# Performance work log

Measured on AMD Instinct MI355X. Metric: run time of the kernel, lower is better.

The kernel has to match this reference:

```python
import jax, jax.numpy as jnp
import numpy as np

N = 50000      # nodes
E = 800000     # edges (before self loops)
IN = 128       # in_channels
H = 4          # heads
C = 32         # hidden_channels (per head)
D = H * C      # concat output dim = 128
NEG_SLOPE = 0.2
LN_EPS = 1e-5


def setup_inputs() -> dict:
    key = jax.random.key(0)
    ks = jax.random.split(key, 24)
    def p(k, shape, s=0.1):
        return jax.random.normal(k, shape, dtype=jnp.float32) * s
    inp = {
        "x": p(ks[0], (N, IN), 1.0),
        "edge_index": jax.random.randint(ks[1], (2, E), 0, N, dtype=jnp.int32),
    }
    i = 2
    for l, ind in [(0, IN), (1, D)]:
        inp[f"Wl{l}"] = p(ks[i], (ind, D)); i += 1
        inp[f"bl{l}"] = p(ks[i], (D,), 0.02); i += 1
        inp[f"Wr{l}"] = p(ks[i], (ind, D)); i += 1
        inp[f"br{l}"] = p(ks[i], (D,), 0.02); i += 1
        inp[f"att{l}"] = p(ks[i], (H, C)); i += 1
        inp[f"Wres{l}"] = p(ks[i], (ind, D)); i += 1
        inp[f"bias{l}"] = p(ks[i], (D,), 0.02); i += 1
        inp[f"g{l}"] = jnp.ones((D,), jnp.float32)
        inp[f"be{l}"] = jnp.zeros((D,), jnp.float32)
    return inp


def _gatv2_layer(x, src, dst, Wl, bl, Wr, br, att, Wres, bias):
    """GATv2Conv with concat heads, add_self_loops already applied, residual."""
    n = x.shape[0]
    xl = (x @ Wl + bl).reshape(n, H, C)   # source transform
    xr = (x @ Wr + br).reshape(n, H, C)   # target transform
    # edge-level attention logits: e = a . LeakyReLU(xl[j] + xr[i])  [E, H]
    eh = jax.nn.leaky_relu(xl[src] + xr[dst], negative_slope=NEG_SLOPE)  # [E,H,C]
    score = jnp.einsum('ehc,hc->eh', eh, att)                            # [E,H]
    # segment softmax over incoming edges of each destination node
    smax = jax.ops.segment_max(score, dst, num_segments=n)               # [N,H]
    ex = jnp.exp(score - smax[dst])
    ssum = jax.ops.segment_sum(ex, dst, num_segments=n)                  # [N,H]
    alpha = ex / ssum[dst]                                               # [E,H]
    msg = xl[src] * alpha[:, :, None]                                    # [E,H,C]
    out = jax.ops.segment_sum(msg, dst, num_segments=n).reshape(n, D)
    return out + x @ Wres + bias  # residual (bias=False linear) + final bias


def _layernorm_relu(x, g, b):
    mu = jnp.mean(x, axis=-1, keepdims=True)
    var = jnp.mean(jnp.square(x - mu), axis=-1, keepdims=True)
    return jax.nn.relu((x - mu) * jax.lax.rsqrt(var + LN_EPS) * g + b)


def reference(x, edge_index,
              Wl0, bl0, Wr0, br0, att0, Wres0, bias0, g0, be0,
              Wl1, bl1, Wr1, br1, att1, Wres1, bias1, g1, be1):
    n = x.shape[0]
    loops = jnp.arange(n, dtype=edge_index.dtype)
    src = jnp.concatenate([edge_index[0], loops])  # add_self_loops=True
    dst = jnp.concatenate([edge_index[1], loops])
    h = _gatv2_layer(x, src, dst, Wl0, bl0, Wr0, br0, att0, Wres0, bias0)
    h = _layernorm_relu(h, g0, be0)
    h = _gatv2_layer(h, src, dst, Wl1, bl1, Wr1, br1, att1, Wres1, bias1)
    h = _layernorm_relu(h, g1, be1)
    return h
```

## Files before the change

kernel.cpp:

```cpp
#include <hip/hip_runtime.h>
#include <math.h>

#define D 128
#define LRELU 0.2f
#define LN_EPS 1e-5f
#define INV_LN2 1.4426950408889634f

#define NBMAX 512
#define CAP 4096
#define P1CHUNK 8192

typedef __attribute__((ext_vector_type(8))) short short8;
typedef __attribute__((ext_vector_type(8))) unsigned short ushort8;
typedef __attribute__((ext_vector_type(4))) float f32x4;
typedef __attribute__((ext_vector_type(2))) float f32x2;
typedef __attribute__((ext_vector_type(2))) unsigned int u32x2;
typedef __attribute__((ext_vector_type(4))) unsigned int u32x4;

static __device__ __forceinline__ unsigned short f2bf(float f) {
    union { float f; unsigned u; } a; a.f = f;
    unsigned r = a.u + 0x7FFFu + ((a.u >> 16) & 1u);
    return (unsigned short)(r >> 16);
}

static __device__ __forceinline__ f32x2 pk_add(f32x2 a, f32x2 b) {
    f32x2 d; asm("v_pk_add_f32 %0, %1, %2" : "=v"(d) : "v"(a), "v"(b)); return d;
}
static __device__ __forceinline__ f32x2 pk_mul(f32x2 a, f32x2 b) {
    f32x2 d; asm("v_pk_mul_f32 %0, %1, %2" : "=v"(d) : "v"(a), "v"(b)); return d;
}
static __device__ __forceinline__ f32x2 pk_fma(f32x2 a, f32x2 b, f32x2 c) {
    f32x2 d; asm("v_pk_fma_f32 %0, %1, %2, %3" : "=v"(d) : "v"(a), "v"(b), "v"(c)); return d;
}
static __device__ __forceinline__ f32x2 pk_abs(f32x2 a) {
    u32x2 u = __builtin_bit_cast(u32x2, a);
    u &= 0x7FFFFFFFu;
    return __builtin_bit_cast(f32x2, u);
}
static __device__ __forceinline__ f32x2 bf2x(unsigned u) {
    f32x2 r;
    r.x = __uint_as_float(u << 16);
    r.y = __uint_as_float(u & 0xFFFF0000u);
    return r;
}

static __device__ __forceinline__ float red4_dpp(float p) {
    int v = __builtin_amdgcn_update_dpp(0, __builtin_bit_cast(int, p), 0xB1, 0xf, 0xf, true);
    p += __builtin_bit_cast(float, v);
    v = __builtin_amdgcn_update_dpp(0, __builtin_bit_cast(int, p), 0x4E, 0xf, 0xf, true);
    p += __builtin_bit_cast(float, v);
    return p;
}

#define SCB 256


__global__ __launch_bounds__(256) void k_prep(
    const int* __restrict__ srcp, const int* __restrict__ dstp,
    int* __restrict__ bcur, unsigned* __restrict__ ebuf, int E, int N,
    const float* __restrict__ X, ushort* __restrict__ Xb, int Mp,
    const float* __restrict__ W0, const float* __restrict__ W1, const float* __restrict__ W2,
    const float* __restrict__ W3, const float* __restrict__ W4, const float* __restrict__ W5,
    ushort* __restrict__ Wp, int nP1, int nCV)
{
    const int bx = blockIdx.x;
    const int tid = threadIdx.x;
    if (bx < nP1) {
        __shared__ int h[NBMAX];
        const int E2 = E + N;
        const int e0 = bx * P1CHUNK;
        const int e1 = min(e0 + P1CHUNK, E2);
        for (int t = tid; t < NBMAX; t += 256) h[t] = 0;
        __syncthreads();
        for (int e = e0 + tid; e < e1; e += 256) {
            int d = (e < E) ? dstp[e] : e - E;
            atomicAdd(&h[d >> 7], 1);
        }
        __syncthreads();
        for (int b = tid; b < NBMAX; b += 256) {
            int c = h[b];
            h[b] = c ? atomicAdd(&bcur[b], c) : 0;
        }
        __syncthreads();
        for (int e = e0 + tid; e < e1; e += 256) {
            int d  = (e < E) ? dstp[e] : e - E;
            int sc = (e < E) ? srcp[e] : e - E;
            int b = d >> 7;
            int pos = atomicAdd(&h[b], 1) & (CAP - 1);
            ebuf[(size_t)b * CAP + pos] = ((unsigned)sc << 7) | (unsigned)(d & 127);
        }
    } else if (bx < nP1 + nCV) {
        int idx = (bx - nP1) * 256 + tid;
        if (idx >= Mp * (D / 4)) return;
        ushort4 o;
        if (idx < N * (D / 4)) {
            float4 v = ((const float4*)X)[idx];
            o.x = f2bf(v.x); o.y = f2bf(v.y); o.z = f2bf(v.z); o.w = f2bf(v.w);
        } else {
            o = make_ushort4(0, 0, 0, 0);
        }
        ((ushort4*)Xb)[idx] = o;
    } else {
        int bid = bx - nP1 - nCV;
        int m = bid >> 6;
        int o = ((bid & 63) << 8) + tid;
        const float* W;
        if (m == 0) W = W0; else if (m == 1) W = W1; else if (m == 2) W = W2;
        else if (m == 3) W = W3; else if (m == 4) W = W4; else W = W5;
        int j  = o & 7;
        int l  = (o >> 3) & 63;
        int ct = (o >> 9) & 7;
        int kc = o >> 12;
        int k   = kc * 32 + ((l >> 4) << 3) + j;
        int col = (ct << 4) + (l & 15);
        Wp[m * 16384 + o] = f2bf(W[k * D + col]);
    }
}


__global__ __launch_bounds__(256) void bhist_kernel(const unsigned* __restrict__ ebuf,
                                                    const int* __restrict__ bcur,
                                                    int* __restrict__ deg,
                                                    int* __restrict__ btot, int N) {
    const int b = blockIdx.x;
    const int base = b << 7;
    const int tid = threadIdx.x;
    __shared__ int h[128];
    __shared__ int t2[2];
    if (tid < 128) h[tid] = 0;
    __syncthreads();
    const int cnt = min(bcur[b], CAP);
    for (int k = tid; k < cnt; k += 256) {
        unsigned v = ebuf[(size_t)b * CAP + k];
        atomicAdd(&h[v & 127], 1);
    }
    __syncthreads();
    int v = (tid < 128) ? h[tid] : 0;
    if (tid < 128 && base + tid < N) deg[base + tid] = v;
    #pragma unroll
    for (int o = 32; o >= 1; o >>= 1) v += __shfl_xor(v, o);
    if (tid == 0)  t2[0] = v;
    if (tid == 64) t2[1] = v;
    __syncthreads();
    if (tid == 0) btot[b] = t2[0] + t2[1];
}


static __device__ __forceinline__ void gemm_body(
    int bxg, int seg, int tid,
    const ushort* __restrict__ Xb, const ushort* __restrict__ Wp,
    const float* __restrict__ bl, const float* __restrict__ br,
    ushort* __restrict__ XLb, ushort* __restrict__ XRb, ushort* __restrict__ RESb)
{
    const int l = tid & 63;
    const int wave = tid >> 6;
    const int wr = wave >> 1, wc = wave & 1;
    const int brow = bxg * 128 + wr * 64;
    const ushort* W = Wp + seg * 16384;

    f32x4 acc[4][4] = {};
    const int arow = brow + (l & 15);
    const int koff = (l >> 4) * 8;

    #pragma unroll
    for (int kc = 0; kc < 4; ++kc) {
        short8 A[4], B[4];
        #pragma unroll
        for (int at = 0; at < 4; ++at)
            A[at] = *(const short8*)&Xb[(size_t)(arow + at * 16) * D + kc * 32 + koff];
        #pragma unroll
        for (int ct = 0; ct < 4; ++ct) {
            int ctg = wc * 4 + ct;
            B[ct] = *(const short8*)&W[(((kc * 8 + ctg) * 64) + l) * 8];
        }
        #pragma unroll
        for (int at = 0; at < 4; ++at)
            #pragma unroll
            for (int ct = 0; ct < 4; ++ct)
                acc[at][ct] = __builtin_amdgcn_mfma_f32_16x16x32_bf16(A[at], B[ct], acc[at][ct], 0, 0, 0);
    }

    const int c = l & 15;
    const int r0 = (l >> 4) * 4;
    const float* bias = (seg == 0) ? bl : ((seg == 1) ? br : nullptr);
    #pragma unroll
    for (int ct = 0; ct < 4; ++ct) {
        int gcol = wc * 64 + ct * 16 + c;
        float bv = bias ? bias[gcol] : 0.f;
        #pragma unroll
        for (int at = 0; at < 4; ++at) {
            #pragma unroll
            for (int r = 0; r < 4; ++r) {
                int grow = brow + at * 16 + r0 + r;
                float v = acc[at][ct][r] + bv;
                size_t off = (size_t)grow * D + gcol;
                if (seg == 0)      XLb[off]  = f2bf(v);
                else if (seg == 1) XRb[off]  = f2bf(v);
                else               RESb[off] = f2bf(v);
            }
        }
    }
}


__global__ __launch_bounds__(256) void k_mid(
    const unsigned* __restrict__ ebuf, const int* __restrict__ bcur,
    const int* __restrict__ deg, const int* __restrict__ btot,
    int* __restrict__ off, int* __restrict__ csrc, int N, int NB, int nblk,
    const ushort* __restrict__ Xb, const ushort* __restrict__ Wp,
    const float* __restrict__ bl, const float* __restrict__ br,
    ushort* __restrict__ XLb, ushort* __restrict__ XRb, ushort* __restrict__ RESb)
{
    const int bx = blockIdx.x;
    if (bx < NB) {
        const int b = bx;
        const int base = b << 7;
        const int tid = threadIdx.x;
        __shared__ int cur[128];
        __shared__ int wsum[4];
        __shared__ int wtot[2];

        int acc = 0;
        for (int t = tid; t < b; t += 256) acc += btot[t];
        #pragma unroll
        for (int o = 32; o >= 1; o >>= 1) acc += __shfl_xor(acc, o);
        if ((tid & 63) == 0) wsum[tid >> 6] = acc;
        __syncthreads();
        const int B = wsum[0] + wsum[1] + wsum[2] + wsum[3];

        int dv = 0;
        if (tid < 128 && base + tid < N) dv = deg[base + tid];
        int incl = dv;
        if (tid < 128) {
            #pragma unroll
            for (int o = 1; o < 64; o <<= 1) {
                int u = __shfl_up(incl, o);
                if ((tid & 63) >= o) incl += u;
            }
        }
        if (tid == 63)  wtot[0] = incl;
        if (tid == 127) wtot[1] = incl;
        __syncthreads();
        if (tid < 128) {
            int add = (tid >= 64) ? wtot[0] : 0;
            int excl = B + add + incl - dv;
            cur[tid] = excl;
            if (base + tid < N) off[base + tid] = excl;
        }
        if (b == NB - 1 && tid == 0) off[N] = B + wtot[0] + wtot[1];
        __syncthreads();

        const int cnt = min(bcur[b], CAP);
        for (int k = tid; k < cnt; k += 256) {
            unsigned v = ebuf[(size_t)b * CAP + k];
            int p = atomicAdd(&cur[v & 127], 1);
            csrc[p] = v >> 7;
        }
    } else {
        int bid = bx - NB;
        int seg = bid / nblk;
        int bxg = bid - seg * nblk;
        gemm_body(bxg, seg, threadIdx.x, Xb, Wp, bl, br, XLb, XRb, RESb);
    }
}

__global__ __launch_bounds__(256) void gemm_mfma(
    const ushort* __restrict__ Xb, const ushort* __restrict__ Wp,
    const float* __restrict__ bl, const float* __restrict__ br,
    ushort* __restrict__ XLb, ushort* __restrict__ XRb, ushort* __restrict__ RESb)
{
    gemm_body(blockIdx.x, blockIdx.y, threadIdx.x, Xb, Wp, bl, br, XLb, XRb, RESb);
}


__global__ __launch_bounds__(256) void gat_node(
    const ushort* __restrict__ XLb, const ushort* __restrict__ XRb, const ushort* __restrict__ RESb,
    const float* __restrict__ att, const float* __restrict__ bias,
    const float* __restrict__ g, const float* __restrict__ be,
    const int* __restrict__ off, const int* __restrict__ csrc,
    float* __restrict__ OUTf, ushort* __restrict__ OUTb)
{
    const int l = threadIdx.x & 63;
    const int i = blockIdx.x * 16 + (threadIdx.x >> 6) * 4 + (l >> 4);
    const int f = (l & 15) * 8;
    const unsigned ibase = ((unsigned)i << 7) + f;
    const int lb = l & 48;

    f32x2 at06[4], at04[4];
    #pragma unroll
    for (int k = 0; k < 4; ++k) {
        float2 a = *(const float2*)&att[f + k * 2];
        f32x2 av; av.x = a.x; av.y = a.y;
        at06[k] = av * (0.6f * INV_LN2);
        at04[k] = av * (0.4f * INV_LN2);
    }

    u32x4 xru = __builtin_nontemporal_load((const u32x4*)&XRb[ibase]);
    f32x2 xr2[4];
    xr2[0] = bf2x(xru.x); xr2[1] = bf2x(xru.y); xr2[2] = bf2x(xru.z); xr2[3] = bf2x(xru.w);

    const int e0 = off[i], e1 = off[i + 1];
    const int len = e1 - e0;
    int mx = max(len, __shfl_xor(len, 16));
    mx = max(mx, __shfl_xor(mx, 32));

    float mA = -1e30f, sA = 0.f;
    float mB = -1e30f, sB = 0.f;
    f32x2 aA[4] = {};
    f32x2 aB[4] = {};

    for (int c0 = 0; c0 < mx; c0 += 16) {
        int myj = __builtin_nontemporal_load(&csrc[min(e0 + c0 + (l & 15), e1 - 1)]);
        const int rem = mx - c0;
        const int nbb = min(4, (rem + 3) >> 2);
        const int kleft = len - c0;

        u32x4 u_[4];
        {
            int s0 = __shfl(myj, lb + 0);
            int s1 = __shfl(myj, lb + 1);
            int s2 = __shfl(myj, lb + 2);
            int s3 = __shfl(myj, lb + 3);
            u_[0] = *(const u32x4*)&XLb[((unsigned)s0 << 7) + f];
            u_[1] = *(const u32x4*)&XLb[((unsigned)s1 << 7) + f];
            u_[2] = *(const u32x4*)&XLb[((unsigned)s2 << 7) + f];
            u_[3] = *(const u32x4*)&XLb[((unsigned)s3 << 7) + f];
        }

        #pragma unroll
        for (int bb = 0; bb < 4; ++bb) {
            if (bb >= nbb) break;
            u32x4 uc[4];
            #pragma unroll
            for (int j = 0; j < 4; ++j) uc[j] = u_[j];
            if (bb + 1 < nbb) {
                int s0 = __shfl(myj, lb + (bb + 1) * 4 + 0);
                int s1 = __shfl(myj, lb + (bb + 1) * 4 + 1);
                int s2 = __shfl(myj, lb + (bb + 1) * 4 + 2);
                int s3 = __shfl(myj, lb + (bb + 1) * 4 + 3);
                u_[0] = *(const u32x4*)&XLb[((unsigned)s0 << 7) + f];
                u_[1] = *(const u32x4*)&XLb[((unsigned)s1 << 7) + f];
                u_[2] = *(const u32x4*)&XLb[((unsigned)s2 << 7) + f];
                u_[3] = *(const u32x4*)&XLb[((unsigned)s3 << 7) + f];
            }

            const int kb = kleft - bb * 4;
            f32x2 xp[4][4];
            float p[4];
            #pragma unroll
            for (int j = 0; j < 4; ++j) {
                xp[j][0] = bf2x(uc[j].x);
                xp[j][1] = bf2x(uc[j].y);
                xp[j][2] = bf2x(uc[j].z);
                xp[j][3] = bf2x(uc[j].w);
                f32x2 v0 = pk_add(xp[j][0], xr2[0]);
                f32x2 pj2 = pk_mul(v0, at06[0]);
                pj2 = pk_fma(pk_abs(v0), at04[0], pj2);
                #pragma unroll
                for (int k = 1; k < 4; ++k) {
                    f32x2 v = pk_add(xp[j][k], xr2[k]);
                    pj2 = pk_fma(v, at06[k], pj2);
                    pj2 = pk_fma(pk_abs(v), at04[k], pj2);
                }
                float pj = pj2.x + pj2.y;
                pj = red4_dpp(pj);
                p[j] = (j < kb) ? pj : -1e30f;
            }
            float m0 = (bb & 1) ? mB : mA;
            float s0v = (bb & 1) ? sB : sA;
            float pmax = fmaxf(fmaxf(p[0], p[1]), fmaxf(p[2], p[3]));
            float nm = fmaxf(m0, pmax);
            float so = exp2f(m0 - nm);
            float w0 = exp2f(p[0] - nm), w1 = exp2f(p[1] - nm);
            float w2 = exp2f(p[2] - nm), w3 = exp2f(p[3] - nm);
            w0 = (0 < kb) ? w0 : 0.f;
            w1 = (1 < kb) ? w1 : 0.f;
            w2 = (2 < kb) ? w2 : 0.f;
            w3 = (3 < kb) ? w3 : 0.f;
            float sn = s0v * so + ((w0 + w1) + (w2 + w3));
            f32x2 so2; so2.x = so; so2.y = so;
            f32x2 w02; w02.x = w0; w02.y = w0;
            f32x2 w12; w12.x = w1; w12.y = w1;
            f32x2 w22; w22.x = w2; w22.y = w2;
            f32x2 w32; w32.x = w3; w32.y = w3;
            if (bb & 1) {
                #pragma unroll
                for (int k = 0; k < 4; ++k) {
                    f32x2 t = pk_mul(xp[0][k], w02);
                    t = pk_fma(xp[1][k], w12, t);
                    t = pk_fma(xp[2][k], w22, t);
                    t = pk_fma(xp[3][k], w32, t);
                    aB[k] = pk_fma(aB[k], so2, t);
                }
                mB = nm; sB = sn;
            } else {
                #pragma unroll
                for (int k = 0; k < 4; ++k) {
                    f32x2 t = pk_mul(xp[0][k], w02);
                    t = pk_fma(xp[1][k], w12, t);
                    t = pk_fma(xp[2][k], w22, t);
                    t = pk_fma(xp[3][k], w32, t);
                    aA[k] = pk_fma(aA[k], so2, t);
                }
                mA = nm; sA = sn;
            }
        }
    }

    float nmv = fmaxf(mA, mB);
    float soA = exp2f(mA - nmv);
    float soB = exp2f(mB - nmv);
    float s = sA * soA + sB * soB;
    f32x2 soA2; soA2.x = soA; soA2.y = soA;
    f32x2 soB2; soB2.x = soB; soB2.y = soB;
    f32x2 a2[4];
    #pragma unroll
    for (int k = 0; k < 4; ++k)
        a2[k] = pk_add(pk_mul(aA[k], soA2), pk_mul(aB[k], soB2));

    u32x4 ru = __builtin_nontemporal_load((const u32x4*)&RESb[ibase]);
    f32x2 rs2[4];
    rs2[0] = bf2x(ru.x); rs2[1] = bf2x(ru.y); rs2[2] = bf2x(ru.z); rs2[3] = bf2x(ru.w);
    const float4 biA = *(const float4*)&bias[f];
    const float4 biB = *(const float4*)&bias[f + 4];
    float inv = 1.f / s;
    float r0 = a2[0].x * inv + rs2[0].x + biA.x;
    float r1 = a2[0].y * inv + rs2[0].y + biA.y;
    float r2 = a2[1].x * inv + rs2[1].x + biA.z;
    float r3 = a2[1].y * inv + rs2[1].y + biA.w;
    float r4 = a2[2].x * inv + rs2[2].x + biB.x;
    float r5 = a2[2].y * inv + rs2[2].y + biB.y;
    float r6 = a2[3].x * inv + rs2[3].x + biB.z;
    float r7 = a2[3].y * inv + rs2[3].y + biB.w;

    float sum = ((r0 + r1) + (r2 + r3)) + ((r4 + r5) + (r6 + r7));
    float sq  = ((r0 * r0 + r1 * r1) + (r2 * r2 + r3 * r3))
              + ((r4 * r4 + r5 * r5) + (r6 * r6 + r7 * r7));
    #pragma unroll
    for (int o = 8; o >= 1; o >>= 1) {
        sum += __shfl_xor(sum, o);
        sq  += __shfl_xor(sq, o);
    }
    float mu  = sum * (1.f / 128.f);
    float var = sq * (1.f / 128.f) - mu * mu;
    float isd = rsqrtf(var + LN_EPS);
    const float4 gvA = *(const float4*)&g[f];
    const float4 gvB = *(const float4*)&g[f + 4];
    const float4 bvA = *(const float4*)&be[f];
    const float4 bvB = *(const float4*)&be[f + 4];
    float o0 = fmaxf((r0 - mu) * isd * gvA.x + bvA.x, 0.f);
    float o1 = fmaxf((r1 - mu) * isd * gvA.y + bvA.y, 0.f);
    float o2 = fmaxf((r2 - mu) * isd * gvA.z + bvA.z, 0.f);
    float o3 = fmaxf((r3 - mu) * isd * gvA.w + bvA.w, 0.f);
    float o4 = fmaxf((r4 - mu) * isd * gvB.x + bvB.x, 0.f);
    float o5 = fmaxf((r5 - mu) * isd * gvB.y + bvB.y, 0.f);
    float o6 = fmaxf((r6 - mu) * isd * gvB.z + bvB.z, 0.f);
    float o7 = fmaxf((r7 - mu) * isd * gvB.w + bvB.w, 0.f);

    if (OUTb) {
        ushort8 ob;
        ob[0] = f2bf(o0); ob[1] = f2bf(o1); ob[2] = f2bf(o2); ob[3] = f2bf(o3);
        ob[4] = f2bf(o4); ob[5] = f2bf(o5); ob[6] = f2bf(o6); ob[7] = f2bf(o7);
        __builtin_nontemporal_store(ob, (ushort8*)&OUTb[ibase]);
    } else {
        f32x4 oA; oA.x = o0; oA.y = o1; oA.z = o2; oA.w = o3;
        f32x4 oB; oB.x = o4; oB.y = o5; oB.z = o6; oB.w = o7;
        __builtin_nontemporal_store(oA, (f32x4*)&OUTf[ibase]);
        __builtin_nontemporal_store(oB, (f32x4*)&OUTf[ibase + 4]);
    }
}


extern "C" void kernel_launch(void* const* d_in, const int* in_sizes, int n_in,
                              void* d_out, int out_size, void* d_ws, size_t ws_size,
                              hipStream_t stream)
{
    const float* x    = (const float*)d_in[0];
    const int*   ei   = (const int*)d_in[1];
    const float* Wl0  = (const float*)d_in[2];
    const float* bl0  = (const float*)d_in[3];
    const float* Wr0  = (const float*)d_in[4];
    const float* br0  = (const float*)d_in[5];
    const float* att0 = (const float*)d_in[6];
    const float* Wres0= (const float*)d_in[7];
    const float* bias0= (const float*)d_in[8];
    const float* g0   = (const float*)d_in[9];
    const float* be0  = (const float*)d_in[10];
    const float* Wl1  = (const float*)d_in[11];
    const float* bl1  = (const float*)d_in[12];
    const float* Wr1  = (const float*)d_in[13];
    const float* br1  = (const float*)d_in[14];
    const float* att1 = (const float*)d_in[15];
    const float* Wres1= (const float*)d_in[16];
    const float* bias1= (const float*)d_in[17];
    const float* g1   = (const float*)d_in[18];
    const float* be1  = (const float*)d_in[19];

    const int N  = in_sizes[0] / D;
    const int E  = in_sizes[1] / 2;
    const int E2 = E + N;
    const int nblk = (N + 127) / 128;
    const int Mp = nblk * 128;
    const int NB = nblk;

    char* w = (char*)d_ws;
    ushort* Xb   = (ushort*)w; w += (size_t)Mp * D * 2;
    ushort* Hb   = (ushort*)w; w += (size_t)Mp * D * 2;
    ushort* XLb  = (ushort*)w; w += (size_t)Mp * D * 2;
    ushort* XRb  = (ushort*)w; w += (size_t)Mp * D * 2;
    ushort* RESb = (ushort*)w; w += (size_t)Mp * D * 2;
    ushort* Wp   = (ushort*)w; w += (size_t)6 * 16384 * 2;
    int* deg     = (int*)w; w += (size_t)N * 4;
    int* off     = (int*)w; w += (size_t)(N + 1) * 4;
    int* bcur    = (int*)w; w += (size_t)NBMAX * 4;
    int* btot    = (int*)w; w += (size_t)NBMAX * 4;
    unsigned* ebuf = (unsigned*)w; w += (size_t)NB * CAP * 4;
    int* csrc    = (int*)w; w += (size_t)E2 * 4;

    const int* srcp = ei;
    const int* dstp = ei + E;

    const int nP1 = (E2 + P1CHUNK - 1) / P1CHUNK;
    const int nCV = (Mp * (D / 4) + 255) / 256;
    const int nPW = 6 * 64;
    const int nGM = nblk * 3;

    hipMemsetAsync(bcur, 0, (size_t)NBMAX * 4, stream);
    k_prep<<<nP1 + nCV + nPW, 256, 0, stream>>>(srcp, dstp, bcur, ebuf, E, N,
                                                x, Xb, Mp,
                                                Wl0, Wr0, Wres0, Wl1, Wr1, Wres1,
                                                Wp, nP1, nCV);
    bhist_kernel<<<NB, 256, 0, stream>>>(ebuf, bcur, deg, btot, N);

    k_mid<<<NB + nGM, 256, 0, stream>>>(ebuf, bcur, deg, btot, off, csrc, N, NB, nblk,
                                        Xb, Wp, bl0, br0, XLb, XRb, RESb);

    const int gatg = N / 16;
    dim3 ggrid(nblk, 3);

    gat_node<<<gatg, 256, 0, stream>>>(XLb, XRb, RESb, att0, bias0, g0, be0, off, csrc, nullptr, Hb);
    gemm_mfma<<<ggrid, 256, 0, stream>>>(Hb, Wp + 3 * 16384, bl1, br1, XLb, XRb, RESb);
    gat_node<<<gatg, 256, 0, stream>>>(XLb, XRb, RESb, att1, bias1, g1, be1, off, csrc, (float*)d_out, nullptr);
}
```

Baseline: 185.1 us.

## Fold bucket histogram into CSR build and merge dual softmax accumulators

Removes the separate bhist_kernel launch. Each k_mid bucket block now builds its own per-node degree histogram from ebuf in shared memory and takes bucket prefix totals straight from bcur, which drops one launch and the deg/btot global round trips. The GAT node kernel also replaces the two alternating online-softmax accumulator sets (A/B) with a single running max/sum/accumulator, cutting registers and the final merge. The trade-off is a longer serial dependency chain in the softmax loop. Prefix sums from bcur ignore the CAP clamp, which differs from before only if a bucket overflows.

```diff
diff --git a/kernel.cpp b/kernel.cpp
--- a/kernel.cpp
+++ b/kernel.cpp
@@ -51,8 +51,6 @@
     p += __builtin_bit_cast(float, v);
     return p;
 }
-
-#define SCB 256
 
 
 __global__ __launch_bounds__(256) void k_prep(
@@ -118,34 +116,6 @@
 }
 
 
-__global__ __launch_bounds__(256) void bhist_kernel(const unsigned* __restrict__ ebuf,
-                                                    const int* __restrict__ bcur,
-                                                    int* __restrict__ deg,
-                                                    int* __restrict__ btot, int N) {
-    const int b = blockIdx.x;
-    const int base = b << 7;
-    const int tid = threadIdx.x;
-    __shared__ int h[128];
-    __shared__ int t2[2];
-    if (tid < 128) h[tid] = 0;
-    __syncthreads();
-    const int cnt = min(bcur[b], CAP);
-    for (int k = tid; k < cnt; k += 256) {
-        unsigned v = ebuf[(size_t)b * CAP + k];
-        atomicAdd(&h[v & 127], 1);
-    }
-    __syncthreads();
-    int v = (tid < 128) ? h[tid] : 0;
-    if (tid < 128 && base + tid < N) deg[base + tid] = v;
-    #pragma unroll
-    for (int o = 32; o >= 1; o >>= 1) v += __shfl_xor(v, o);
-    if (tid == 0)  t2[0] = v;
-    if (tid == 64) t2[1] = v;
-    __syncthreads();
-    if (tid == 0) btot[b] = t2[0] + t2[1];
-}
-
-
 static __device__ __forceinline__ void gemm_body(
     int bxg, int seg, int tid,
     const ushort* __restrict__ Xb, const ushort* __restrict__ Wp,
@@ -205,7 +175,6 @@
 
 __global__ __launch_bounds__(256) void k_mid(
     const unsigned* __restrict__ ebuf, const int* __restrict__ bcur,
-    const int* __restrict__ deg, const int* __restrict__ btot,
     int* __restrict__ off, int* __restrict__ csrc, int N, int NB, int nblk,
     const ushort* __restrict__ Xb, const ushort* __restrict__ Wp,
     const float* __restrict__ bl, const float* __restrict__ br,
@@ -216,20 +185,29 @@
         const int b = bx;
         const int base = b << 7;
         const int tid = threadIdx.x;
+        const int cntN = min(128, N - base);
+        __shared__ int h[128];
         __shared__ int cur[128];
         __shared__ int wsum[4];
         __shared__ int wtot[2];
 
         int acc = 0;
-        for (int t = tid; t < b; t += 256) acc += btot[t];
+        for (int t = tid; t < b; t += 256) acc += bcur[t];
         #pragma unroll
         for (int o = 32; o >= 1; o >>= 1) acc += __shfl_xor(acc, o);
         if ((tid & 63) == 0) wsum[tid >> 6] = acc;
+        if (tid < 128) h[tid] = 0;
         __syncthreads();
         const int B = wsum[0] + wsum[1] + wsum[2] + wsum[3];
 
-        int dv = 0;
-        if (tid < 128 && base + tid < N) dv = deg[base + tid];
+        const int cnt = min(bcur[b], CAP);
+        for (int k = tid; k < cnt; k += 256) {
+            unsigned v = ebuf[(size_t)b * CAP + k];
+            atomicAdd(&h[v & 127], 1);
+        }
+        __syncthreads();
+
+        int dv = (tid < 128) ? h[tid] : 0;
         int incl = dv;
         if (tid < 128) {
             #pragma unroll
@@ -245,12 +223,11 @@
             int add = (tid >= 64) ? wtot[0] : 0;
             int excl = B + add + incl - dv;
             cur[tid] = excl;
-            if (base + tid < N) off[base + tid] = excl;
+            if (tid < cntN) off[base + tid] = excl;
         }
         if (b == NB - 1 && tid == 0) off[N] = B + wtot[0] + wtot[1];
         __syncthreads();
 
-        const int cnt = min(bcur[b], CAP);
         for (int k = tid; k < cnt; k += 256) {
             unsigned v = ebuf[(size_t)b * CAP + k];
             int p = atomicAdd(&cur[v & 127], 1);
@@ -304,10 +281,8 @@
     int mx = max(len, __shfl_xor(len, 16));
     mx = max(mx, __shfl_xor(mx, 32));
 
-    float mA = -1e30f, sA = 0.f;
-    float mB = -1e30f, sB = 0.f;
-    f32x2 aA[4] = {};
-    f32x2 aB[4] = {};
+    float m = -1e30f, s = 0.f;
+    f32x2 a2[4] = {};
 
     for (int c0 = 0; c0 < mx; c0 += 16) {
         int myj = __builtin_nontemporal_load(&csrc[min(e0 + c0 + (l & 15), e1 - 1)]);
@@ -366,57 +341,28 @@
                 pj = red4_dpp(pj);
                 p[j] = (j < kb) ? pj : -1e30f;
             }
-            float m0 = (bb & 1) ? mB : mA;
-            float s0v = (bb & 1) ? sB : sA;
             float pmax = fmaxf(fmaxf(p[0], p[1]), fmaxf(p[2], p[3]));
-            float nm = fmaxf(m0, pmax);
-            float so = exp2f(m0 - nm);
+            float nm = fmaxf(m, pmax);
+            float so = exp2f(m - nm);
             float w0 = exp2f(p[0] - nm), w1 = exp2f(p[1] - nm);
             float w2 = exp2f(p[2] - nm), w3 = exp2f(p[3] - nm);
-            w0 = (0 < kb) ? w0 : 0.f;
-            w1 = (1 < kb) ? w1 : 0.f;
-            w2 = (2 < kb) ? w2 : 0.f;
-            w3 = (3 < kb) ? w3 : 0.f;
-            float sn = s0v * so + ((w0 + w1) + (w2 + w3));
+            s = s * so + ((w0 + w1) + (w2 + w3));
             f32x2 so2; so2.x = so; so2.y = so;
             f32x2 w02; w02.x = w0; w02.y = w0;
             f32x2 w12; w12.x = w1; w12.y = w1;
             f32x2 w22; w22.x = w2; w22.y = w2;
             f32x2 w32; w32.x = w3; w32.y = w3;
-            if (bb & 1) {
-                #pragma unroll
-                for (int k = 0; k < 4; ++k) {
-                    f32x2 t = pk_mul(xp[0][k], w02);
-                    t = pk_fma(xp[1][k], w12, t);
-                    t = pk_fma(xp[2][k], w22, t);
-                    t = pk_fma(xp[3][k], w32, t);
-                    aB[k] = pk_fma(aB[k], so2, t);
-                }
-                mB = nm; sB = sn;
-            } else {
-                #pragma unroll
-                for (int k = 0; k < 4; ++k) {
-                    f32x2 t = pk_mul(xp[0][k], w02);
-                    t = pk_fma(xp[1][k], w12, t);
-                    t = pk_fma(xp[2][k], w22, t);
-                    t = pk_fma(xp[3][k], w32, t);
-                    aA[k] = pk_fma(aA[k], so2, t);
-                }
-                mA = nm; sA = sn;
+            #pragma unroll
+            for (int k = 0; k < 4; ++k) {
+                f32x2 t = pk_mul(xp[0][k], w02);
+                t = pk_fma(xp[1][k], w12, t);
+                t = pk_fma(xp[2][k], w22, t);
+                t = pk_fma(xp[3][k], w32, t);
+                a2[k] = pk_fma(a2[k], so2, t);
             }
-        }
-    }
-
-    float nmv = fmaxf(mA, mB);
-    float soA = exp2f(mA - nmv);
-    float soB = exp2f(mB - nmv);
-    float s = sA * soA + sB * soB;
-    f32x2 soA2; soA2.x = soA; soA2.y = soA;
-    f32x2 soB2; soB2.x = soB; soB2.y = soB;
-    f32x2 a2[4];
-    #pragma unroll
-    for (int k = 0; k < 4; ++k)
-        a2[k] = pk_add(pk_mul(aA[k], soA2), pk_mul(aB[k], soB2));
+            m = nm;
+        }
+    }
 
     u32x4 ru = __builtin_nontemporal_load((const u32x4*)&RESb[ibase]);
     f32x2 rs2[4];
@@ -510,10 +456,8 @@
     ushort* XRb  = (ushort*)w; w += (size_t)Mp * D * 2;
     ushort* RESb = (ushort*)w; w += (size_t)Mp * D * 2;
     ushort* Wp   = (ushort*)w; w += (size_t)6 * 16384 * 2;
-    int* deg     = (int*)w; w += (size_t)N * 4;
     int* off     = (int*)w; w += (size_t)(N + 1) * 4;
     int* bcur    = (int*)w; w += (size_t)NBMAX * 4;
-    int* btot    = (int*)w; w += (size_t)NBMAX * 4;
     unsigned* ebuf = (unsigned*)w; w += (size_t)NB * CAP * 4;
     int* csrc    = (int*)w; w += (size_t)E2 * 4;
 
@@ -530,9 +474,8 @@
                                                 x, Xb, Mp,
                                                 Wl0, Wr0, Wres0, Wl1, Wr1, Wres1,
                                                 Wp, nP1, nCV);
-    bhist_kernel<<<NB, 256, 0, stream>>>(ebuf, bcur, deg, btot, N);
-
-    k_mid<<<NB + nGM, 256, 0, stream>>>(ebuf, bcur, deg, btot, off, csrc, N, NB, nblk,
+
+    k_mid<<<NB + nGM, 256, 0, stream>>>(ebuf, bcur, off, csrc, N, NB, nblk,
                                         Xb, Wp, bl0, br0, XLb, XRb, RESb);
 
     const int gatg = N / 16;
```

New measurement: 177.0 us. 4.4% less time.
